# Performance work log

Measured on AMD Instinct MI355X. Metric: run time of the kernel, lower is better.

## Reference

```python
import math
import jax, jax.numpy as jnp
import numpy as np

N_HEAD = 16

def setup_inputs() -> dict:
    key = jax.random.key(0)
    k1, k2, k3 = jax.random.split(key, 3)
    B, T, C = 2, 2048, 1024
    x = jax.random.normal(k1, (B, T, C), dtype=jnp.float32)
    w_attn = jax.random.normal(k2, (C, 3 * C), dtype=jnp.float32) * (1.0 / math.sqrt(C))
    b_attn = jnp.zeros((3 * C,), dtype=jnp.float32)
    w_proj = jax.random.normal(k3, (C, C), dtype=jnp.float32) * (1.0 / math.sqrt(C))
    b_proj = jnp.zeros((C,), dtype=jnp.float32)
    return {"x": x, "w_attn": w_attn, "b_attn": b_attn, "w_proj": w_proj, "b_proj": b_proj}

def reference(x, w_attn, b_attn, w_proj, b_proj):
    B, T, C = x.shape
    H = N_HEAD
    D = C // H
    qkv = x @ w_attn + b_attn                       # [B,T,3C]
    q, k, v = jnp.split(qkv, 3, axis=-1)
    # [B,T,C] -> [B,H,T,D]
    q = q.reshape(B, T, H, D).transpose(0, 2, 1, 3)
    k = k.reshape(B, T, H, D).transpose(0, 2, 1, 3)
    v = v.reshape(B, T, H, D).transpose(0, 2, 1, 3)
    scores = jnp.einsum("bhtd,bhsd->bhts", q, k) * (1.0 / math.sqrt(D))  # [B,H,T,T]
    causal = jnp.tril(jnp.ones((T, T), dtype=bool))
    scores = jnp.where(causal, scores, jnp.finfo(scores.dtype).min)
    attn = jax.nn.softmax(scores, axis=-1)
    y = jnp.einsum("bhts,bhsd->bhtd", attn, v)      # [B,H,T,D]
    y = y.transpose(0, 2, 1, 3).reshape(B, T, C)
    return y @ w_proj + b_proj
```

## Files before the change

### kernel.cpp

```cpp
#include <hip/hip_runtime.h>
#include <stdint.h>

#define BB 2
#define TT 2048
#define CCx 1024
#define HH 16
#define DD 64
#define MM (BB*TT)
#define C3 (3*CCx)

using u16 = unsigned short;
typedef __attribute__((ext_vector_type(8))) short short8;
typedef __attribute__((ext_vector_type(4))) float f32x4;

__device__ __forceinline__ float bf2f(u16 u){
  union { unsigned int i; float f; } v; v.i = ((unsigned int)u) << 16; return v.f;
}
__device__ __forceinline__ u16 f2bf(float f){
  union { float f; unsigned int u; } v; v.f = f;
  unsigned int r = v.u + 0x7fffu + ((v.u >> 16) & 1u);
  return (u16)(r >> 16);
}

__device__ __forceinline__ f32x4 mfma16x16x32(short8 a, short8 b, f32x4 c){
  return __builtin_amdgcn_mfma_f32_16x16x32_bf16(a, b, c, 0, 0, 0);
}

typedef __attribute__((address_space(1))) unsigned int gu32;
typedef __attribute__((address_space(3))) unsigned int su32;
__device__ __forceinline__ void gload16(const void* g, void* l){
  __builtin_amdgcn_global_load_lds((gu32*)g, (su32*)l, 16, 0, 0);
}

template<int CTRL>
__device__ __forceinline__ float dpp_mov(float x){
  int xi = __builtin_bit_cast(int, x);
  int yi = __builtin_amdgcn_update_dpp(xi, xi, CTRL, 0xF, 0xF, true);
  return __builtin_bit_cast(float, yi);
}
__device__ __forceinline__ float dpp_max16(float x){
  x = fmaxf(x, dpp_mov<0xB1>(x));
  x = fmaxf(x, dpp_mov<0x4E>(x));
  x = fmaxf(x, dpp_mov<0x124>(x));
  x = fmaxf(x, dpp_mov<0x128>(x));
  return x;
}
__device__ __forceinline__ float dpp_sum16(float x){
  x += dpp_mov<0xB1>(x);
  x += dpp_mov<0x4E>(x);
  x += dpp_mov<0x124>(x);
  x += dpp_mov<0x128>(x);
  return x;
}

__global__ __launch_bounds__(256) void cvt_x_k(const float* __restrict__ inv,
                                               u16* __restrict__ out, int n8){
  int i = blockIdx.x*256 + threadIdx.x;
  if (i >= n8) return;
  const float* p = inv + (size_t)i*8;
  float4 a = *(const float4*)p, b = *(const float4*)(p+4);
  short8 v;
  v[0]=(short)f2bf(a.x); v[1]=(short)f2bf(a.y); v[2]=(short)f2bf(a.z); v[3]=(short)f2bf(a.w);
  v[4]=(short)f2bf(b.x); v[5]=(short)f2bf(b.y); v[6]=(short)f2bf(b.z); v[7]=(short)f2bf(b.w);
  *(short8*)(out + (size_t)i*8) = v;
}

__global__ __launch_bounds__(256) void transpose_cvt_k(const float* __restrict__ inv,
                                                       u16* __restrict__ out,
                                                       int R, int Cc){
  __shared__ u16 t[64][65];
  const int bx = blockIdx.x*64, by = blockIdx.y*64;
  const int tx = threadIdx.x & 63, ty = threadIdx.x >> 6;
  #pragma unroll
  for (int i = 0; i < 16; ++i){
    int r = ty + i*4;
    t[r][tx] = f2bf(inv[(size_t)(by+r)*Cc + bx+tx]);
  }
  __syncthreads();
  #pragma unroll
  for (int i = 0; i < 16; ++i){
    int r = ty + i*4;
    out[(size_t)(bx+r)*R + by+tx] = t[tx][r];
  }
}

__global__ __launch_bounds__(512) void gemm_nt(const u16* __restrict__ A,
                                               const u16* __restrict__ BT,
                                               const float* __restrict__ bias,
                                               void* __restrict__ Cmat,
                                               int M, int N, int K, int of32){
  __shared__ u16 lA[128*64];
  __shared__ u16 lB[128*64];
  const int tid  = threadIdx.x;
  const int lane = tid & 63;
  const int wave = tid >> 6;
  const int nwg = gridDim.x * gridDim.y;
  const int lin = blockIdx.y * gridDim.x + blockIdx.x;
  const int wg  = (lin & 7) * (nwg >> 3) + (lin >> 3);
  const int bm = wg % gridDim.x, bn = wg / gridDim.x;
  const int wm = (wave & 3) * 32;
  const int wn = (wave >> 2) * 64;
  const int ln15 = lane & 15, g = lane >> 4;

  f32x4 acc[2][4];
  #pragma unroll
  for (int i = 0; i < 2; ++i)
    #pragma unroll
    for (int j = 0; j < 4; ++j) acc[i][j] = (f32x4){0.f,0.f,0.f,0.f};

  const int trow = tid >> 3;
  const int tc8s = (tid & 7) ^ (trow & 7);
  const size_t arow0 = (size_t)(bm*128) * K;
  const size_t brow0 = (size_t)(bn*128) * K;

  for (int k0 = 0; k0 < K; k0 += 64) {
    __syncthreads();
    #pragma unroll
    for (int c = 0; c < 2; ++c) {
      const int row = c*64 + trow;
      const size_t roff = (size_t)row*K + k0 + tc8s*8;
      char* da = (char*)lA + c*8192 + (wave<<10);
      char* db = (char*)lB + c*8192 + (wave<<10);
      gload16(A + arow0 + roff, da);
      gload16(BT + brow0 + roff, db);
    }
    asm volatile("s_waitcnt vmcnt(0)" ::: "memory");
    __syncthreads();

    short8 af[2][2], bfr[4][2];
    #pragma unroll
    for (int mf = 0; mf < 2; ++mf)
      #pragma unroll
      for (int kc = 0; kc < 2; ++kc) {
        const int r = wm + mf*16 + ln15;
        const int cb = (kc*64 + (g << 4)) ^ ((r & 7) << 4);
        af[mf][kc] = *(const short8*)((const char*)lA + r*128 + cb);
      }
    #pragma unroll
    for (int nf = 0; nf < 4; ++nf)
      #pragma unroll
      for (int kc = 0; kc < 2; ++kc) {
        const int r = wn + nf*16 + ln15;
        const int cb = (kc*64 + (g << 4)) ^ ((r & 7) << 4);
        bfr[nf][kc] = *(const short8*)((const char*)lB + r*128 + cb);
      }
    #pragma unroll
    for (int kc = 0; kc < 2; ++kc)
      #pragma unroll
      for (int mf = 0; mf < 2; ++mf)
        #pragma unroll
        for (int nf = 0; nf < 4; ++nf)
          acc[mf][nf] = mfma16x16x32(af[mf][kc], bfr[nf][kc], acc[mf][nf]);
  }

  #pragma unroll
  for (int nf = 0; nf < 4; ++nf) {
    const int col = bn*128 + wn + nf*16 + ln15;
    const float bv = bias[col];
    #pragma unroll
    for (int mf = 0; mf < 2; ++mf) {
      #pragma unroll
      for (int r = 0; r < 4; ++r) {
        const int rowg = bm*128 + wm + mf*16 + g*4 + r;
        const float v = acc[mf][nf][r] + bv;
        if (of32) ((float*)Cmat)[(size_t)rowg*N + col] = v;
        else      ((u16*)Cmat)[(size_t)rowg*N + col] = f2bf(v);
      }
    }
  }
}

#define LOG2E_S 0.1803369f
__global__ __launch_bounds__(512) void attn_k(const u16* __restrict__ qkv,
                                              u16* __restrict__ y){
  __shared__ u16 kb[2][64*64];
  __shared__ u16 vb[2][64*64];
  __shared__ u16 pls[8][16*64];
  const int tid  = threadIdx.x;
  const int lane = tid & 63;
  const int wave = tid >> 6;
  const int bx = blockIdx.x;
  const int jb = (bx < 8) ? bx : (23 - bx);
  const int bh = blockIdx.y;
  const int b = bh >> 4, h = bh & 15;
  const int ln15 = lane & 15, g = lane >> 4;
  const int sub = wave >> 2;
  const int wq  = wave & 3;
  const int jq  = sub ? (31 - jb) : jb;
  const int q0  = jq*64 + wq*16;
  const int ntw = sub ? (32 - jb) : (jb + 1);
  const int nt  = 32 - jb;
  const size_t base = (size_t)b * TT * C3;

  const int srow = tid >> 3;
  const int sc8  = tid & 7;
  const u16* ksrc0 = qkv + base + CCx + h*DD + (((sc8) ^ (srow & 7)) * 8);
  const u16* vsrc0 = qkv + base + 2*CCx + h*DD + sc8*8;
  char* plw = (char*)pls[wave];

  short8 qf[2];
  {
    const u16* qp = qkv + base + (size_t)(q0 + ln15)*C3 + h*DD + g*8;
    qf[0] = *(const short8*)qp;
    qf[1] = *(const short8*)(qp + 32);
  }

  f32x4 o[4]; float m[4], lsum[4];
  #pragma unroll
  for (int i = 0; i < 4; ++i){ o[i] = (f32x4){0.f,0.f,0.f,0.f}; m[i] = -1e30f; lsum[i] = 0.f; }

  short8 vreg;
  #define VSTORE(curb) do { \
    char* vd_ = (char*)vb + (curb)*8192; \
    _Pragma("unroll") \
    for (int i = 0; i < 8; ++i){ \
      const int d_ = sc8*8 + i; \
      const int sw_ = (i + sc8) & 7; \
      *(u16*)(vd_ + d_*128 + (((srow>>3) ^ sw_) << 4) + (srow & 7)*2) = (u16)vreg[i]; \
    } \
  } while(0)

  gload16(ksrc0 + (size_t)srow*C3, (char*)kb[0] + wave*1024);
  vreg = *(const short8*)(vsrc0 + (size_t)srow*C3);
  asm volatile("s_waitcnt vmcnt(0)" ::: "memory");
  VSTORE(0);
  __syncthreads();

  int cur = 0;
  for (int t = 0; t < nt; ++t){
    const int kv0 = t*64;
    const bool hn = (t + 1 < nt);
    if (hn){
      gload16(ksrc0 + (size_t)(kv0 + 64 + srow)*C3, (char*)kb[cur^1] + wave*1024);
      vreg = *(const short8*)(vsrc0 + (size_t)(kv0 + 64 + srow)*C3);
    }

    if (t < ntw){
      const char* kbc = (const char*)kb + cur*8192;
      f32x4 s[4];
      __builtin_amdgcn_s_setprio(1);
      #pragma unroll
      for (int kf = 0; kf < 4; ++kf){
        const int krow = kf*16 + ln15;
        short8 k0 = *(const short8*)(kbc + krow*128 + ((g*16)      ^ ((krow & 7)*16)));
        short8 k1 = *(const short8*)(kbc + krow*128 + ((64 + g*16) ^ ((krow & 7)*16)));
        f32x4 z = (f32x4){0.f,0.f,0.f,0.f};
        s[kf] = mfma16x16x32(qf[0], k0, z);
        s[kf] = mfma16x16x32(qf[1], k1, s[kf]);
      }
      __builtin_amdgcn_s_setprio(0);

      float tmax[4] = {-1e30f,-1e30f,-1e30f,-1e30f};
      #pragma unroll
      for (int kf = 0; kf < 4; ++kf){
        const int key = kv0 + kf*16 + ln15;
        #pragma unroll
        for (int r = 0; r < 4; ++r){
          const int q = q0 + g*4 + r;
          float v = (key <= q) ? s[kf][r] : -1e30f;
          s[kf][r] = v;
          tmax[r] = fmaxf(tmax[r], v);
        }
      }
      #pragma unroll
      for (int r = 0; r < 4; ++r) tmax[r] = dpp_max16(tmax[r]);
      bool need = false;
      #pragma unroll
      for (int r = 0; r < 4; ++r) need |= (tmax[r] > m[r] + 64.f);
      if (__any(need)){
        #pragma unroll
        for (int r = 0; r < 4; ++r){
          const float nm = fmaxf(m[r], tmax[r]);
          const float fac = exp2f((m[r] - nm) * LOG2E_S);
          m[r] = nm; lsum[r] *= fac;
          #pragma unroll
          for (int db = 0; db < 4; ++db) o[db][r] *= fac;
        }
      }
      float mm[4], rsum[4];
      #pragma unroll
      for (int r = 0; r < 4; ++r){ mm[r] = m[r]*LOG2E_S; rsum[r] = 0.f; }
      #pragma unroll
      for (int r = 0; r < 4; ++r){
        const int qr = g*4 + r;
        char* rowp = plw + qr*128;
        const int swz = qr & 7;
        #pragma unroll
        for (int pk = 0; pk < 2; ++pk){
          const float pa_ = exp2f(fmaf(s[2*pk][r],   LOG2E_S, -mm[r]));
          const float pb_ = exp2f(fmaf(s[2*pk+1][r], LOG2E_S, -mm[r]));
          rsum[r] += pa_ + pb_;
          unsigned w;
          asm("v_cvt_pk_bf16_f32 %0, %1, %2" : "=v"(w) : "v"(pa_), "v"(pb_));
          const int hi8 = ln15 >> 3, lo7 = (ln15 & 7)*2;
          *(u16*)(rowp + (((4*pk   + hi8) ^ swz) << 4) + lo7) = (u16)w;
          *(u16*)(rowp + (((4*pk+2 + hi8) ^ swz) << 4) + lo7) = (u16)(w >> 16);
        }
      }
      #pragma unroll
      for (int r = 0; r < 4; ++r) lsum[r] += dpp_sum16(rsum[r]);
      asm volatile("s_waitcnt lgkmcnt(0)" ::: "memory");
      __builtin_amdgcn_sched_barrier(0);

      const char* vbc = (const char*)vb + cur*8192;
      __builtin_amdgcn_s_setprio(1);
      #pragma unroll
      for (int kc = 0; kc < 2; ++kc){
        const int ch = kc*4 + g;
        short8 pa = *(const short8*)(plw + ln15*128 + ((ch ^ (ln15 & 7)) << 4));
        #pragma unroll
        for (int db = 0; db < 4; ++db){
          const int vd = db*16 + ln15;
          const int swv = ((vd & 7) + ((vd >> 3) & 7)) & 7;
          short8 vbr = *(const short8*)(vbc + vd*128 + ((ch ^ swv) << 4));
          o[db] = mfma16x16x32(pa, vbr, o[db]);
        }
      }
      __builtin_amdgcn_s_setprio(0);
    }

    if (hn){
      asm volatile("s_waitcnt vmcnt(0)" ::: "memory");
      VSTORE(cur^1);
    }
    __syncthreads();
    cur ^= 1;
  }

  float inv[4];
  #pragma unroll
  for (int r = 0; r < 4; ++r) inv[r] = 1.0f / lsum[r];
  #pragma unroll
  for (int db = 0; db < 4; ++db){
    #pragma unroll
    for (int r = 0; r < 4; ++r){
      y[(size_t)(b*TT + q0 + g*4 + r)*CCx + h*DD + db*16 + ln15] = f2bf(o[db][r] * inv[r]);
    }
  }
  #undef VSTORE
}

extern "C" void kernel_launch(void* const* d_in, const int* in_sizes, int n_in,
                              void* d_out, int out_size, void* d_ws, size_t ws_size,
                              hipStream_t stream) {
  const float *x = nullptr, *w_attn = nullptr, *b_attn = nullptr,
              *w_proj = nullptr, *b_proj = nullptr;
  for (int i = 0; i < n_in; ++i) {
    switch (in_sizes[i]) {
      case MM*CCx:  x      = (const float*)d_in[i]; break;
      case C3*CCx:  w_attn = (const float*)d_in[i]; break;
      case C3:      b_attn = (const float*)d_in[i]; break;
      case CCx*CCx: w_proj = (const float*)d_in[i]; break;
      case CCx:     b_proj = (const float*)d_in[i]; break;
    }
  }
  float* out = (float*)d_out;

  char* ws = (char*)d_ws;
  u16* xb      = (u16*)ws;
  u16* wT_attn = xb + (size_t)MM*CCx;
  u16* wT_proj = wT_attn + (size_t)C3*CCx;
  u16* qkv     = wT_proj + (size_t)CCx*CCx;
  u16* ybuf    = qkv + (size_t)MM*C3;

  cvt_x_k<<<(MM*CCx/8 + 255)/256, 256, 0, stream>>>(x, xb, MM*CCx/8);
  transpose_cvt_k<<<dim3(C3/64, CCx/64), 256, 0, stream>>>(w_attn, wT_attn, CCx, C3);
  transpose_cvt_k<<<dim3(CCx/64, CCx/64), 256, 0, stream>>>(w_proj, wT_proj, CCx, CCx);
  gemm_nt<<<dim3(MM/128, C3/128), 512, 0, stream>>>(xb, wT_attn, b_attn, qkv, MM, C3, CCx, 0);
  attn_k<<<dim3(16, BB*HH), 512, 0, stream>>>(qkv, ybuf);
  gemm_nt<<<dim3(MM/128, CCx/128), 512, 0, stream>>>(ybuf, wT_proj, b_proj, out, MM, CCx, CCx, 1);
}
```

Before: 143.7 us.

## Fuse prep kernels into one launch and defer softmax reductions in attention

```diff
diff --git a/kernel.cpp b/kernel.cpp
--- a/kernel.cpp
+++ b/kernel.cpp
@@ -53,24 +53,36 @@
   return x;
 }
 
-__global__ __launch_bounds__(256) void cvt_x_k(const float* __restrict__ inv,
-                                               u16* __restrict__ out, int n8){
-  int i = blockIdx.x*256 + threadIdx.x;
-  if (i >= n8) return;
-  const float* p = inv + (size_t)i*8;
-  float4 a = *(const float4*)p, b = *(const float4*)(p+4);
-  short8 v;
-  v[0]=(short)f2bf(a.x); v[1]=(short)f2bf(a.y); v[2]=(short)f2bf(a.z); v[3]=(short)f2bf(a.w);
-  v[4]=(short)f2bf(b.x); v[5]=(short)f2bf(b.y); v[6]=(short)f2bf(b.z); v[7]=(short)f2bf(b.w);
-  *(short8*)(out + (size_t)i*8) = v;
-}
-
-__global__ __launch_bounds__(256) void transpose_cvt_k(const float* __restrict__ inv,
-                                                       u16* __restrict__ out,
-                                                       int R, int Cc){
+__global__ __launch_bounds__(256) void prep_k(const float* __restrict__ x,
+                                              u16* __restrict__ xb,
+                                              const float* __restrict__ w_attn,
+                                              u16* __restrict__ wT_attn,
+                                              const float* __restrict__ w_proj,
+                                              u16* __restrict__ wT_proj){
   __shared__ u16 t[64][65];
-  const int bx = blockIdx.x*64, by = blockIdx.y*64;
-  const int tx = threadIdx.x & 63, ty = threadIdx.x >> 6;
+  const int bid = blockIdx.x;
+  const int tid = threadIdx.x;
+  if (bid < 2048){
+    const int i = bid*256 + tid;
+    const float* p = x + (size_t)i*8;
+    float4 a = *(const float4*)p, b = *(const float4*)(p+4);
+    short8 v;
+    v[0]=(short)f2bf(a.x); v[1]=(short)f2bf(a.y); v[2]=(short)f2bf(a.z); v[3]=(short)f2bf(a.w);
+    v[4]=(short)f2bf(b.x); v[5]=(short)f2bf(b.y); v[6]=(short)f2bf(b.z); v[7]=(short)f2bf(b.w);
+    *(short8*)(xb + (size_t)i*8) = v;
+    return;
+  }
+  const float* inv; u16* out; int R, Cc, bx, by;
+  if (bid < 2048 + 768){
+    const int b2 = bid - 2048;
+    inv = w_attn; out = wT_attn; R = CCx; Cc = C3;
+    bx = (b2 % 48)*64; by = (b2 / 48)*64;
+  } else {
+    const int b3 = bid - 2816;
+    inv = w_proj; out = wT_proj; R = CCx; Cc = CCx;
+    bx = (b3 % 16)*64; by = (b3 / 16)*64;
+  }
+  const int tx = tid & 63, ty = tid >> 6;
   #pragma unroll
   for (int i = 0; i < 16; ++i){
     int r = ty + i*4;
@@ -119,10 +131,8 @@
     for (int c = 0; c < 2; ++c) {
       const int row = c*64 + trow;
       const size_t roff = (size_t)row*K + k0 + tc8s*8;
-      char* da = (char*)lA + c*8192 + (wave<<10);
-      char* db = (char*)lB + c*8192 + (wave<<10);
-      gload16(A + arow0 + roff, da);
-      gload16(BT + brow0 + roff, db);
+      gload16(A + arow0 + roff, (char*)lA + c*8192 + (wave<<10));
+      gload16(BT + brow0 + roff, (char*)lB + c*8192 + (wave<<10));
     }
     asm volatile("s_waitcnt vmcnt(0)" ::: "memory");
     __syncthreads();
@@ -205,9 +215,9 @@
     qf[1] = *(const short8*)(qp + 32);
   }
 
-  f32x4 o[4]; float m[4], lsum[4];
-  #pragma unroll
-  for (int i = 0; i < 4; ++i){ o[i] = (f32x4){0.f,0.f,0.f,0.f}; m[i] = -1e30f; lsum[i] = 0.f; }
+  f32x4 o[4]; float m[4], plsum[4];
+  #pragma unroll
+  for (int i = 0; i < 4; ++i){ o[i] = (f32x4){0.f,0.f,0.f,0.f}; m[i] = -1e30f; plsum[i] = 0.f; }
 
   short8 vreg;
   #define VSTORE(curb) do { \
@@ -251,35 +261,42 @@
       __builtin_amdgcn_s_setprio(0);
 
       float tmax[4] = {-1e30f,-1e30f,-1e30f,-1e30f};
-      #pragma unroll
-      for (int kf = 0; kf < 4; ++kf){
-        const int key = kv0 + kf*16 + ln15;
-        #pragma unroll
-        for (int r = 0; r < 4; ++r){
-          const int q = q0 + g*4 + r;
-          float v = (key <= q) ? s[kf][r] : -1e30f;
-          s[kf][r] = v;
-          tmax[r] = fmaxf(tmax[r], v);
+      if (t == ntw - 1){
+        #pragma unroll
+        for (int kf = 0; kf < 4; ++kf){
+          const int key = kv0 + kf*16 + ln15;
+          #pragma unroll
+          for (int r = 0; r < 4; ++r){
+            const int q = q0 + g*4 + r;
+            float v = (key <= q) ? s[kf][r] : -1e30f;
+            s[kf][r] = v;
+            tmax[r] = fmaxf(tmax[r], v);
+          }
         }
-      }
-      #pragma unroll
-      for (int r = 0; r < 4; ++r) tmax[r] = dpp_max16(tmax[r]);
+      } else {
+        #pragma unroll
+        for (int kf = 0; kf < 4; ++kf)
+          #pragma unroll
+          for (int r = 0; r < 4; ++r)
+            tmax[r] = fmaxf(tmax[r], s[kf][r]);
+      }
       bool need = false;
       #pragma unroll
       for (int r = 0; r < 4; ++r) need |= (tmax[r] > m[r] + 64.f);
       if (__any(need)){
         #pragma unroll
         for (int r = 0; r < 4; ++r){
-          const float nm = fmaxf(m[r], tmax[r]);
+          const float tr = dpp_max16(tmax[r]);
+          const float nm = fmaxf(m[r], tr);
           const float fac = exp2f((m[r] - nm) * LOG2E_S);
-          m[r] = nm; lsum[r] *= fac;
+          m[r] = nm; plsum[r] *= fac;
           #pragma unroll
           for (int db = 0; db < 4; ++db) o[db][r] *= fac;
         }
       }
-      float mm[4], rsum[4];
-      #pragma unroll
-      for (int r = 0; r < 4; ++r){ mm[r] = m[r]*LOG2E_S; rsum[r] = 0.f; }
+      float mm[4];
+      #pragma unroll
+      for (int r = 0; r < 4; ++r) mm[r] = m[r]*LOG2E_S;
       #pragma unroll
       for (int r = 0; r < 4; ++r){
         const int qr = g*4 + r;
@@ -289,7 +306,7 @@
         for (int pk = 0; pk < 2; ++pk){
           const float pa_ = exp2f(fmaf(s[2*pk][r],   LOG2E_S, -mm[r]));
           const float pb_ = exp2f(fmaf(s[2*pk+1][r], LOG2E_S, -mm[r]));
-          rsum[r] += pa_ + pb_;
+          plsum[r] += pa_ + pb_;
           unsigned w;
           asm("v_cvt_pk_bf16_f32 %0, %1, %2" : "=v"(w) : "v"(pa_), "v"(pb_));
           const int hi8 = ln15 >> 3, lo7 = (ln15 & 7)*2;
@@ -297,8 +314,6 @@
           *(u16*)(rowp + (((4*pk+2 + hi8) ^ swz) << 4) + lo7) = (u16)(w >> 16);
         }
       }
-      #pragma unroll
-      for (int r = 0; r < 4; ++r) lsum[r] += dpp_sum16(rsum[r]);
       asm volatile("s_waitcnt lgkmcnt(0)" ::: "memory");
       __builtin_amdgcn_sched_barrier(0);
 
@@ -329,7 +344,7 @@
 
   float inv[4];
   #pragma unroll
-  for (int r = 0; r < 4; ++r) inv[r] = 1.0f / lsum[r];
+  for (int r = 0; r < 4; ++r) inv[r] = 1.0f / dpp_sum16(plsum[r]);
   #pragma unroll
   for (int db = 0; db < 4; ++db){
     #pragma unroll
@@ -363,9 +378,7 @@
   u16* qkv     = wT_proj + (size_t)CCx*CCx;
   u16* ybuf    = qkv + (size_t)MM*C3;
 
-  cvt_x_k<<<(MM*CCx/8 + 255)/256, 256, 0, stream>>>(x, xb, MM*CCx/8);
-  transpose_cvt_k<<<dim3(C3/64, CCx/64), 256, 0, stream>>>(w_attn, wT_attn, CCx, C3);
-  transpose_cvt_k<<<dim3(CCx/64, CCx/64), 256, 0, stream>>>(w_proj, wT_proj, CCx, CCx);
+  prep_k<<<3072, 256, 0, stream>>>(x, xb, w_attn, wT_attn, w_proj, wT_proj);
   gemm_nt<<<dim3(MM/128, C3/128), 512, 0, stream>>>(xb, wT_attn, b_attn, qkv, MM, C3, CCx, 0);
   attn_k<<<dim3(16, BB*HH), 512, 0, stream>>>(qkv, ybuf);
   gemm_nt<<<dim3(MM/128, CCx/128), 512, 0, stream>>>(ybuf, wT_proj, b_proj, out, MM, CCx, CCx, 1);
```

Result: faster. 127.8 us, median of 2 (-11.1%).
